# Kernel optimization log

Measured on AMD Instinct MI355X. Metric: run time of the kernel, lower is better.

Reference implementation:

```python
import jax, jax.numpy as jnp
import numpy as np

# Mamba2 dims (match init_kwargs)
DM = 1024          # d_model
EXPAND = 2
D_INNER = EXPAND * DM            # 2048 (== d_ssm)
HEADDIM = 64
NHEADS = D_INNER // HEADDIM      # 32
DSTATE = 128
NGROUPS = 1
DCONV = 4
CONV_DIM = D_INNER + 2 * NGROUPS * DSTATE        # 2304
D_IN_PROJ = 2 * D_INNER + 2 * NGROUPS * DSTATE + NHEADS  # 4384
BATCH, SEQ = 4, 1024
EPS = 1e-5


def setup_inputs() -> dict:
    key = jax.random.key(0)
    ks = jax.random.split(key, 8)
    x = jax.random.normal(ks[0], (BATCH, SEQ, DM), dtype=jnp.float32)
    in_proj_w = jax.random.normal(ks[1], (D_IN_PROJ, DM), dtype=jnp.float32) * 0.02
    conv_w = jax.random.normal(ks[2], (CONV_DIM, 1, DCONV), dtype=jnp.float32) * 0.2
    conv_b = jnp.zeros((CONV_DIM,), dtype=jnp.float32)
    # dt_bias = inv_softplus(dt) with dt ~ logU[dt_min, dt_max]
    dt = jnp.exp(jax.random.uniform(ks[3], (NHEADS,)) * (np.log(0.1) - np.log(0.001)) + np.log(0.001))
    dt_bias = dt + jnp.log(-jnp.expm1(-dt))
    # A ~ U[1, 16], A_log = log(A)
    A_log = jnp.log(jax.random.uniform(ks[4], (NHEADS,), minval=1.0, maxval=16.0))
    D = jnp.ones((NHEADS,), dtype=jnp.float32)
    norm_w = jnp.ones((D_INNER,), dtype=jnp.float32)
    out_proj_w = jax.random.normal(ks[5], (DM, D_INNER), dtype=jnp.float32) * 0.02
    return {"x": x, "in_proj_w": in_proj_w, "conv_w": conv_w, "conv_b": conv_b,
            "dt_bias": dt_bias, "A_log": A_log, "D": D, "norm_w": norm_w,
            "out_proj_w": out_proj_w}


def _mamba2_forward(x, in_proj_w, conv_w, conv_b, dt_bias, A_log, D, norm_w, out_proj_w):
    B, L, _ = x.shape
    zxbcdt = jnp.einsum('bld,ed->ble', x, in_proj_w)  # (B,L,D_IN_PROJ)
    z = zxbcdt[..., :D_INNER]
    xBC = zxbcdt[..., D_INNER:D_INNER + CONV_DIM]
    dt_raw = zxbcdt[..., D_INNER + CONV_DIM:]         # (B,L,NHEADS)

    # causal depthwise conv1d + silu
    xt = jnp.transpose(xBC, (0, 2, 1))                # (B, CONV_DIM, L)
    conv = jax.lax.conv_general_dilated(
        xt, conv_w, window_strides=(1,), padding=[(DCONV - 1, 0)],
        dimension_numbers=('NCH', 'OIH', 'NCH'), feature_group_count=CONV_DIM)
    conv = conv + conv_b[None, :, None]
    xBC = jnp.transpose(jax.nn.silu(conv), (0, 2, 1))  # (B,L,CONV_DIM)

    x_ssm = xBC[..., :D_INNER].reshape(B, L, NHEADS, HEADDIM)
    Bm = xBC[..., D_INNER:D_INNER + NGROUPS * DSTATE].reshape(B, L, NGROUPS, DSTATE)
    Cm = xBC[..., D_INNER + NGROUPS * DSTATE:].reshape(B, L, NGROUPS, DSTATE)

    dt = jax.nn.softplus(dt_raw + dt_bias)            # (B,L,H)
    A = -jnp.exp(A_log)                               # (H,)
    dA = jnp.exp(dt * A)                              # (B,L,H)
    dtx = dt[..., None] * x_ssm                       # (B,L,H,P)

    rep = NHEADS // NGROUPS
    Bh = jnp.repeat(Bm, rep, axis=2)                  # (B,L,H,N)
    Ch = jnp.repeat(Cm, rep, axis=2)

    def step(h, inp):
        dA_t, dtx_t, B_t, C_t = inp
        h = dA_t[:, :, None, None] * h + dtx_t[..., None] * B_t[:, :, None, :]
        y = jnp.einsum('bhpn,bhn->bhp', h, C_t)
        return h, y

    h0 = jnp.zeros((B, NHEADS, HEADDIM, DSTATE), dtype=x.dtype)
    xs = (jnp.transpose(dA, (1, 0, 2)),
          jnp.transpose(dtx, (1, 0, 2, 3)),
          jnp.transpose(Bh, (1, 0, 2, 3)),
          jnp.transpose(Ch, (1, 0, 2, 3)))
    _, ys = jax.lax.scan(step, h0, xs)                # (L,B,H,P)
    y = jnp.transpose(ys, (1, 0, 2, 3)) + D[None, None, :, None] * x_ssm
    y = y.reshape(B, L, D_INNER)

    # gated RMSNorm (norm_before_gate=False): normalize(y * silu(z)) * w
    yz = y * jax.nn.silu(z)
    yz = yz * jax.lax.rsqrt(jnp.mean(yz * yz, axis=-1, keepdims=True) + EPS) * norm_w

    return jnp.einsum('bld,ed->ble', yz, out_proj_w)  # (B,L,DM)


def reference(x, in_proj_w, conv_w, conv_b, dt_bias, A_log, D, norm_w, out_proj_w):
    return _mamba2_forward(x, in_proj_w, conv_w, conv_b, dt_bias, A_log, D, norm_w, out_proj_w)
```

## Files before the change

### kernel.cpp

```cpp
#include <hip/hip_runtime.h>
#include <hip/hip_bf16.h>

#define DM        1024
#define D_INNER   2048
#define NHEADS    32
#define HEADDIM   64
#define DSTATE    128
#define DCONV     4
#define CONV_DIM  (D_INNER + 2*DSTATE)
#define D_IN_PROJ (2*D_INNER + 2*DSTATE + NHEADS)
#define NPAD_IN   4480
#define BATCH     4
#define SEQ       1024
#define NROWS     (BATCH*SEQ)
#define EPSF      1e-5f
#define CHUNK     128
#define NCHUNK    (SEQ/CHUNK)
#define BH        (BATCH*NHEADS)

#define OFF_ZX   ((size_t)0)
#define OFF_XBC  ((size_t)(NROWS)*D_IN_PROJ)
#define OFF_DT   (OFF_XBC + (size_t)NROWS*CONV_DIM)
#define OFF_DA   (OFF_DT  + (size_t)NROWS*NHEADS)
#define OFF_Y    (OFF_DA  + (size_t)NROWS*NHEADS)
#define FLOAT_END (OFF_Y + (size_t)NROWS*D_INNER)
#define SOFF_XB   ((size_t)0)
#define SOFF_W1B  (SOFF_XB  + (size_t)NROWS*DM)
#define SOFF_W2B  (SOFF_W1B + (size_t)NPAD_IN*DM)
#define SOFF_YZB  (SOFF_W2B + (size_t)DM*D_INNER)
#define HD_SHORTS ((size_t)NCHUNK*BH*HEADDIM*DSTATE)

typedef float  vf4   __attribute__((ext_vector_type(4)));
typedef short  s16x8 __attribute__((ext_vector_type(8)));
typedef short  s16x4 __attribute__((ext_vector_type(4)));
typedef __bf16 bf16x8 __attribute__((ext_vector_type(8)));

__device__ __forceinline__ float sigmoidf_(float x) { return 1.f / (1.f + expf(-x)); }

__device__ __forceinline__ short f2bf(float f) {
    unsigned u = __builtin_bit_cast(unsigned, f);
    u += 0x7fffu + ((u >> 16) & 1u);
    return (short)(u >> 16);
}
__device__ __forceinline__ float bf2f(short s) {
    unsigned u = ((unsigned)(unsigned short)s) << 16;
    return __builtin_bit_cast(float, u);
}
__device__ __forceinline__ bf16x8 as_bf(s16x8 v) { return __builtin_bit_cast(bf16x8, v); }
#define MFMA(a,b,c) __builtin_amdgcn_mfma_f32_16x16x32_bf16(as_bf(a), as_bf(b), (c), 0, 0, 0)

template <typename T> __device__ __forceinline__ T cvt_out(float v);
template <> __device__ __forceinline__ float cvt_out<float>(float v) { return v; }
template <> __device__ __forceinline__ short cvt_out<short>(float v) { return f2bf(v); }

__device__ __forceinline__ void gload16(const short* g, short* l) {
    __builtin_amdgcn_global_load_lds(
        (const __attribute__((address_space(1))) unsigned int*)g,
        (__attribute__((address_space(3))) unsigned int*)l, 16, 0, 0);
}

__device__ __forceinline__ int swz_idx(int r, int kc) {
    return r * 128 + (((kc) ^ (r & 7)) << 3);
}
__device__ __forceinline__ int swz64_idx(int r, int c) {
    return r * 64 + (((c) ^ (r & 7)) << 3);
}
__device__ __forceinline__ void stage_tile(const float* __restrict__ g, int gstride,
                                           short* __restrict__ lds, int rows,
                                           int tid, int nthr) {
    for (int s = tid; s < rows * 16; s += nthr) {
        int r = s >> 4, c = s & 15;
        const float* p = g + (size_t)r * gstride + c * 8;
        float4 v0 = *(const float4*)p, v1 = *(const float4*)(p + 4);
        s16x8 o;
        o[0]=f2bf(v0.x); o[1]=f2bf(v0.y); o[2]=f2bf(v0.z); o[3]=f2bf(v0.w);
        o[4]=f2bf(v1.x); o[5]=f2bf(v1.y); o[6]=f2bf(v1.z); o[7]=f2bf(v1.w);
        *(s16x8*)&lds[swz_idx(r, c)] = o;
    }
}

__global__ __launch_bounds__(256) void cvt_bf16(const float* __restrict__ src,
                                                short* __restrict__ dst,
                                                int n_src, int n_dst) {
    int i = (blockIdx.x * 256 + threadIdx.x) * 4;
    if (i >= n_dst) return;
    s16x4 o;
    if (i + 3 < n_src) {
        float4 v = *(const float4*)(src + i);
        o[0] = f2bf(v.x); o[1] = f2bf(v.y); o[2] = f2bf(v.z); o[3] = f2bf(v.w);
    } else {
        #pragma unroll
        for (int j = 0; j < 4; ++j) o[j] = (i + j < n_src) ? f2bf(src[i + j]) : (short)0;
    }
    *(s16x4*)(dst + i) = o;
}

template <typename OutT>
__global__ __launch_bounds__(256) void gemm_mfma(const short* __restrict__ A,
                                                 const short* __restrict__ B,
                                                 OutT* __restrict__ C,
                                                 int K, int Nout, int nbx) {
    __shared__ short smem[16384];
    const int tid = threadIdx.x;
    const int cpx = gridDim.x >> 3;
    const int wgid = (blockIdx.x & 7) * cpx + (blockIdx.x >> 3);
    const int bm = (wgid / nbx) * 128, bn = (wgid % nbx) * 128;
    const int lane = tid & 63, lr = lane & 15, lg = lane >> 4;
    const int w = tid >> 6, wm = w >> 1, wn = w & 1;

    const short* ga[4]; const short* gb[4];
    short* la[4]; short* lb[4];
    #pragma unroll
    for (int t = 0; t < 4; ++t) {
        int s = t * 256 + tid;
        int r = s >> 3;
        int c = (s & 7) ^ (r & 7);
        ga[t] = A + (size_t)(bm + r) * K + c * 8;
        gb[t] = B + (size_t)(bn + r) * K + c * 8;
        la[t] = &smem[s * 8];
        lb[t] = &smem[8192 + s * 8];
    }

    vf4 acc[4][4] = {};

    for (int k0 = 0; k0 < K; k0 += 64) {
        __syncthreads();
        #pragma unroll
        for (int t = 0; t < 4; ++t) gload16(ga[t] + k0, la[t]);
        #pragma unroll
        for (int t = 0; t < 4; ++t) gload16(gb[t] + k0, lb[t]);
        __syncthreads();
        #pragma unroll
        for (int kk = 0; kk < 2; ++kk) {
            const int co = ((kk * 4 + lg) ^ (lr & 7)) * 8;
            s16x8 av[4], bv[4];
            #pragma unroll
            for (int f = 0; f < 4; ++f) {
                av[f] = *(const s16x8*)&smem[(wm * 64 + f * 16 + lr) * 64 + co];
                bv[f] = *(const s16x8*)&smem[8192 + (wn * 64 + f * 16 + lr) * 64 + co];
            }
            #pragma unroll
            for (int i = 0; i < 4; ++i)
                #pragma unroll
                for (int j = 0; j < 4; ++j)
                    acc[i][j] = MFMA(av[i], bv[j], acc[i][j]);
        }
    }

    #pragma unroll
    for (int i = 0; i < 4; ++i) {
        int row = bm + wm * 64 + i * 16 + lg * 4;
        #pragma unroll
        for (int j = 0; j < 4; ++j) {
            int col = bn + wn * 64 + j * 16 + lr;
            if (col < Nout) {
                OutT* cp = C + (size_t)row * Nout + col;
                #pragma unroll
                for (int q = 0; q < 4; ++q) cp[(size_t)q * Nout] = cvt_out<OutT>(acc[i][j][q]);
            }
        }
    }
}

__global__ __launch_bounds__(256) void conv_silu(const short* __restrict__ zx,
                                                 const float* __restrict__ cw,
                                                 const float* __restrict__ cb,
                                                 float* __restrict__ xBC) {
    int idx = blockIdx.x * 256 + threadIdx.x;
    if (idx >= NROWS * CONV_DIM) return;
    int c  = idx % CONV_DIM;
    int bl = idx / CONV_DIM;
    int b  = bl / SEQ;
    int l  = bl % SEQ;

    float w0 = cw[c*4+0], w1 = cw[c*4+1], w2 = cw[c*4+2], w3 = cw[c*4+3];
    const short* base = zx + (size_t)b * SEQ * D_IN_PROJ + D_INNER + c;

    float acc = cb[c];
    if (l >= 3) acc = fmaf(bf2f(base[(size_t)(l-3) * D_IN_PROJ]), w0, acc);
    if (l >= 2) acc = fmaf(bf2f(base[(size_t)(l-2) * D_IN_PROJ]), w1, acc);
    if (l >= 1) acc = fmaf(bf2f(base[(size_t)(l-1) * D_IN_PROJ]), w2, acc);
    acc = fmaf(bf2f(base[(size_t)l * D_IN_PROJ]), w3, acc);

    xBC[idx] = acc * sigmoidf_(acc);
}

__global__ __launch_bounds__(256) void dt_da(const short* __restrict__ zx,
                                             const float* __restrict__ dt_bias,
                                             float* __restrict__ dt) {
    int idx = blockIdx.x * 256 + threadIdx.x;
    if (idx >= NROWS * NHEADS) return;
    int h  = idx & (NHEADS - 1);
    int bl = idx >> 5;
    float u = bf2f(zx[(size_t)bl * D_IN_PROJ + D_INNER + CONV_DIM + h]) + dt_bias[h];
    float d = (u > 20.f) ? u : log1pf(expf(u));
    dt[idx] = d;
}

#define L_CT 0
#define L_XT 0
#define L_BT 16384
#define L_BW 32768
#define L_XN 49152
__global__ __launch_bounds__(1024) void ssm_mfma_a(const float* __restrict__ xBC,
                                                   const float* __restrict__ dt,
                                                   const float* __restrict__ A_log,
                                                   const float* __restrict__ Dp,
                                                   float* __restrict__ y,
                                                   short* __restrict__ hd16,
                                                   float* __restrict__ datot) {
    __shared__ short sm[57344];
    __shared__ float dtl[128], lcs[128];
    int blk = (blockIdx.x & 7) * (gridDim.x >> 3) + (blockIdx.x >> 3);
    int h = blk & 31, k = (blk >> 5) & (NCHUNK - 1), b = blk >> 8;
    int tid = threadIdx.x, w = tid >> 6, lane = tid & 63, lr = lane & 15, lg = lane >> 4;
    int bl0 = b * SEQ + k * CHUNK;
    const float* xrow = xBC + (size_t)bl0 * CONV_DIM;

    if (tid < 128) dtl[tid] = dt[(size_t)(bl0 + tid) * NHEADS + h];

    stage_tile(xrow + D_INNER + DSTATE, CONV_DIM, sm + L_CT, 128, tid, 1024);
    stage_tile(xrow + D_INNER,          CONV_DIM, sm + L_BT, 128, tid, 1024);
    {
        int r = tid >> 3, c = tid & 7;
        const float* p = xrow + (size_t)r * CONV_DIM + h * HEADDIM + c * 8;
        float4 v0 = *(const float4*)p, v1 = *(const float4*)(p + 4);
        s16x8 o;
        o[0]=f2bf(v0.x); o[1]=f2bf(v0.y); o[2]=f2bf(v0.z); o[3]=f2bf(v0.w);
        o[4]=f2bf(v1.x); o[5]=f2bf(v1.y); o[6]=f2bf(v1.z); o[7]=f2bf(v1.w);
        *(s16x8*)&sm[L_XN + swz64_idx(r, c)] = o;
    }
    __syncthreads();

    float Ah = -__expf(A_log[h]);
    if (w == 0) {
        float a = dtl[lane], bb = dtl[64 + lane];
        #pragma unroll
        for (int d = 1; d < 64; d <<= 1) { float v = __shfl_up(a, d);  if (lane >= d) a  += v; }
        #pragma unroll
        for (int d = 1; d < 64; d <<= 1) { float v = __shfl_up(bb, d); if (lane >= d) bb += v; }
        bb += __shfl(a, 63);
        lcs[lane]      = Ah * a;
        lcs[64 + lane] = Ah * bb;
        if (lane == 63) datot[k * BH + b * NHEADS + h] = __expf(Ah * bb);
    }

    vf4 g[4] = {};
    const int rb = (w & 7) * 16, cb = (w >> 3) * 64;
    #pragma unroll
    for (int ks = 0; ks < 4; ++ks) {
        int kc = ks * 4 + lg;
        s16x8 av = *(const s16x8*)&sm[L_CT + swz_idx(rb + lr, kc)];
        #pragma unroll
        for (int jf = 0; jf < 4; ++jf) {
            s16x8 bv = *(const s16x8*)&sm[L_BT + swz_idx(cb + jf * 16 + lr, kc)];
            g[jf] = MFMA(av, bv, g[jf]);
        }
    }
    __syncthreads();

    float lcLast = lcs[127];

    {
        int p = tid & 63, c2 = tid >> 6;
        s16x8 o;
        #pragma unroll
        for (int jj = 0; jj < 8; ++jj) {
            int j = c2 * 8 + jj;
            float xv = bf2f(sm[L_XN + swz64_idx(j, p >> 3) + (p & 7)]);
            o[jj] = f2bf(dtl[j] * xv);
        }
        *(s16x8*)&sm[L_XT + swz_idx(p, c2)] = o;
    }
    for (int s = tid; s < 2048; s += 1024) {
        int n = s & 127, c = s >> 7;
        s16x8 o;
        #pragma unroll
        for (int jj = 0; jj < 8; ++jj) {
            int j = c * 8 + jj;
            float bv = bf2f(sm[L_BT + swz_idx(j, n >> 3) + (n & 7)]);
            o[jj] = f2bf(bv * __expf(lcLast - lcs[j]));
        }
        *(s16x8*)&sm[L_BW + swz_idx(n, c)] = o;
    }
    __syncthreads();

    #pragma unroll
    for (int jf = 0; jf < 4; ++jf)
        #pragma unroll
        for (int q = 0; q < 4; ++q) {
            int t = rb + lg * 4 + q;
            int j = cb + jf * 16 + lr;
            float v = (j <= t) ? g[jf][q] * __expf(lcs[t] - lcs[j]) : 0.f;
            sm[L_BT + swz_idx(t, j >> 3) + (j & 7)] = f2bf(v);
        }
    __syncthreads();

    vf4 yi[2] = {};
    vf4 hdl[2] = {};
    const int rb2 = (w & 7) * 16, prb = (w >> 3) * 32;
    const int hrb = (w & 3) * 16, hcb = (w >> 2) * 32;
    #pragma unroll
    for (int ks = 0; ks < 4; ++ks) {
        int kc = ks * 4 + lg;
        s16x8 am = *(const s16x8*)&sm[L_BT + swz_idx(rb2 + lr, kc)];
        s16x8 ax = *(const s16x8*)&sm[L_XT + swz_idx(hrb + lr, kc)];
        #pragma unroll
        for (int jf = 0; jf < 2; ++jf) {
            s16x8 bx = *(const s16x8*)&sm[L_XT + swz_idx(prb + jf * 16 + lr, kc)];
            s16x8 bw = *(const s16x8*)&sm[L_BW + swz_idx(hcb + jf * 16 + lr, kc)];
            yi[jf]  = MFMA(am, bx, yi[jf]);
            hdl[jf] = MFMA(ax, bw, hdl[jf]);
        }
    }

    float Dh = Dp[h];
    #pragma unroll
    for (int jf = 0; jf < 2; ++jf)
        #pragma unroll
        for (int q = 0; q < 4; ++q) {
            int t = rb2 + lg * 4 + q;
            int p = prb + jf * 16 + lr;
            float xv = xrow[(size_t)t * CONV_DIM + h * HEADDIM + p];
            y[(size_t)(bl0 + t) * D_INNER + h * HEADDIM + p] = yi[jf][q] + Dh * xv;
        }
    size_t hb = ((size_t)k * BH + b * NHEADS + h) * (HEADDIM * DSTATE);
    #pragma unroll
    for (int jf = 0; jf < 2; ++jf)
        #pragma unroll
        for (int q = 0; q < 4; ++q) {
            int p = hrb + lg * 4 + q;
            int n = hcb + jf * 16 + lr;
            hd16[hb + p * DSTATE + n] = f2bf(hdl[jf][q]);
        }
}

__global__ __launch_bounds__(512) void ssm_state_b(short* __restrict__ hd16,
                                                   const float* __restrict__ datot) {
    int bh = blockIdx.x;
    int base = threadIdx.x * 16;
    float hs[16];
    #pragma unroll
    for (int i = 0; i < 16; ++i) hs[i] = 0.f;
    #pragma unroll
    for (int k = 0; k < NCHUNK; ++k) {
        size_t off = ((size_t)k * BH + bh) * (HEADDIM * DSTATE) + base;
        float da = datot[k * BH + bh];
        s16x8 d0 = *(const s16x8*)&hd16[off], d1 = *(const s16x8*)&hd16[off + 8];
        s16x8 o0, o1;
        #pragma unroll
        for (int i = 0; i < 8; ++i) { o0[i] = f2bf(hs[i]); o1[i] = f2bf(hs[8 + i]); }
        *(s16x8*)&hd16[off] = o0; *(s16x8*)&hd16[off + 8] = o1;
        #pragma unroll
        for (int i = 0; i < 8; ++i) {
            hs[i]     = fmaf(da, hs[i],     bf2f(d0[i]));
            hs[8 + i] = fmaf(da, hs[8 + i], bf2f(d1[i]));
        }
    }
}

__global__ __launch_bounds__(512) void ssm_mfma_c(const float* __restrict__ xBC,
                                                  const float* __restrict__ dt,
                                                  const float* __restrict__ A_log,
                                                  const short* __restrict__ hd16,
                                                  float* __restrict__ y) {
    int blk = (blockIdx.x & 7) * (gridDim.x >> 3) + (blockIdx.x >> 3);
    int h = blk & 31, k = (blk >> 5) & (NCHUNK - 1), b = blk >> 8;
    if (k == 0) return;
    __shared__ short sm[16384];
    __shared__ float dtl[128], lcs[128];
    int tid = threadIdx.x, w = tid >> 6, lane = tid & 63, lr = lane & 15, lg = lane >> 4;
    int bl0 = b * SEQ + k * CHUNK;
    const float* xrow = xBC + (size_t)bl0 * CONV_DIM;

    if (tid < 128) dtl[tid] = dt[(size_t)(bl0 + tid) * NHEADS + h];
    __syncthreads();
    stage_tile(xrow + D_INNER + DSTATE, CONV_DIM, sm, 128, tid, 512);
    float Ah = -__expf(A_log[h]);
    __syncthreads();
    if (w == 0) {
        float a = dtl[lane], bb = dtl[64 + lane];
        #pragma unroll
        for (int d = 1; d < 64; d <<= 1) { float v = __shfl_up(a, d);  if (lane >= d) a  += v; }
        #pragma unroll
        for (int d = 1; d < 64; d <<= 1) { float v = __shfl_up(bb, d); if (lane >= d) bb += v; }
        bb += __shfl(a, 63);
        lcs[lane]      = Ah * a;
        lcs[64 + lane] = Ah * bb;
    }
    __syncthreads();

    const short* hin = hd16 + ((size_t)k * BH + b * NHEADS + h) * (HEADDIM * DSTATE);
    vf4 yi[2][2] = {};
    const int rb = (w & 3) * 32, prb = (w >> 2) * 32;
    #pragma unroll
    for (int ks = 0; ks < 4; ++ks) {
        int kc = ks * 4 + lg;
        s16x8 av[2], bv[2];
        #pragma unroll
        for (int i = 0; i < 2; ++i)  { int r = rb + i * 16 + lr; av[i] = *(const s16x8*)&sm[swz_idx(r, kc)]; }
        #pragma unroll
        for (int jf = 0; jf < 2; ++jf){
            int p = prb + jf * 16 + lr;
            bv[jf] = *(const s16x8*)&hin[p * DSTATE + ks * 32 + lg * 8];
        }
        #pragma unroll
        for (int i = 0; i < 2; ++i)
            #pragma unroll
            for (int jf = 0; jf < 2; ++jf)
                yi[i][jf] = MFMA(av[i], bv[jf], yi[i][jf]);
    }
    #pragma unroll
    for (int i = 0; i < 2; ++i)
        #pragma unroll
        for (int jf = 0; jf < 2; ++jf)
            #pragma unroll
            for (int q = 0; q < 4; ++q) {
                int t = rb + i * 16 + lg * 4 + q;
                int p = prb + jf * 16 + lr;
                float* yp = y + (size_t)(bl0 + t) * D_INNER + h * HEADDIM + p;
                *yp = fmaf(__expf(lcs[t]), yi[i][jf][q], *yp);
            }
}

__global__ __launch_bounds__(256) void gate_rmsnorm(const float* __restrict__ y,
                                                    const short* __restrict__ zxs,
                                                    const float* __restrict__ nw,
                                                    short* __restrict__ yzb) {
    int bl = blockIdx.x;
    const float* yr = y + (size_t)bl * D_INNER;
    const short* zr = zxs + (size_t)bl * D_IN_PROJ;
    int e0 = threadIdx.x * 8;

    float4 y0 = *(const float4*)(yr + e0);
    float4 y1 = *(const float4*)(yr + e0 + 4);
    s16x8 zv = *(const s16x8*)(zr + e0);

    float v[8];
    float yy[8] = {y0.x, y0.y, y0.z, y0.w, y1.x, y1.y, y1.z, y1.w};
    float ss = 0.f;
    #pragma unroll
    for (int i = 0; i < 8; ++i) {
        float zz = bf2f(zv[i]);
        v[i] = yy[i] * zz * sigmoidf_(zz);
        ss = fmaf(v[i], v[i], ss);
    }
    ss += __shfl_xor(ss, 1);  ss += __shfl_xor(ss, 2);  ss += __shfl_xor(ss, 4);
    ss += __shfl_xor(ss, 8);  ss += __shfl_xor(ss, 16); ss += __shfl_xor(ss, 32);
    __shared__ float red[4];
    int wave = threadIdx.x >> 6;
    if ((threadIdx.x & 63) == 0) red[wave] = ss;
    __syncthreads();
    ss = red[0] + red[1] + red[2] + red[3];

    float scale = rsqrtf(ss * (1.f / D_INNER) + EPSF);
    s16x8 o;
    #pragma unroll
    for (int i = 0; i < 8; ++i) o[i] = f2bf(v[i] * scale * nw[e0 + i]);
    *(s16x8*)(yzb + (size_t)bl * D_INNER + e0) = o;
}

extern "C" void kernel_launch(void* const* d_in, const int* in_sizes, int n_in,
                              void* d_out, int out_size, void* d_ws, size_t ws_size,
                              hipStream_t stream) {
    const float* x        = (const float*)d_in[0];
    const float* in_w     = (const float*)d_in[1];
    const float* conv_w   = (const float*)d_in[2];
    const float* conv_b   = (const float*)d_in[3];
    const float* dt_bias  = (const float*)d_in[4];
    const float* A_log    = (const float*)d_in[5];
    const float* Dp       = (const float*)d_in[6];
    const float* norm_w   = (const float*)d_in[7];
    const float* out_w    = (const float*)d_in[8];
    float* out            = (float*)d_out;

    float* ws   = (float*)d_ws;
    short* zxs  = (short*)(ws + OFF_ZX);
    float* xBC  = ws + OFF_XBC;
    float* dt   = ws + OFF_DT;
    float* y    = ws + OFF_Y;
    short* sb   = (short*)(ws + FLOAT_END);
    short* xb   = sb + SOFF_XB;
    short* w1b  = sb + SOFF_W1B;
    short* w2b  = sb + SOFF_W2B;
    short* yzb  = sb + SOFF_YZB;
    short* hd16  = xb;
    float* datot = (float*)(hd16 + HD_SHORTS);

    {
        int n = NROWS * DM;
        cvt_bf16<<<n / 4 / 256, 256, 0, stream>>>(x, xb, n, n);
        int ns = D_IN_PROJ * DM, nd = NPAD_IN * DM;
        cvt_bf16<<<nd / 4 / 256, 256, 0, stream>>>(in_w, w1b, ns, nd);
        int n2 = DM * D_INNER;
        cvt_bf16<<<n2 / 4 / 256, 256, 0, stream>>>(out_w, w2b, n2, n2);
    }
    gemm_mfma<short><<<(NPAD_IN / 128) * (NROWS / 128), 256, 0, stream>>>(
        xb, w1b, zxs, DM, D_IN_PROJ, NPAD_IN / 128);
    {
        int total = NROWS * CONV_DIM;
        conv_silu<<<(total + 255) / 256, 256, 0, stream>>>(zxs, conv_w, conv_b, xBC);
    }
    {
        int total = NROWS * NHEADS;
        dt_da<<<(total + 255) / 256, 256, 0, stream>>>(zxs, dt_bias, dt);
    }
    ssm_mfma_a<<<BATCH * NCHUNK * NHEADS, 1024, 0, stream>>>(xBC, dt, A_log, Dp, y, hd16, datot);
    ssm_state_b<<<BH, 512, 0, stream>>>(hd16, datot);
    ssm_mfma_c<<<BATCH * NCHUNK * NHEADS, 512, 0, stream>>>(xBC, dt, A_log, hd16, y);
    gate_rmsnorm<<<NROWS, 256, 0, stream>>>(y, zxs, norm_w, yzb);
    gemm_mfma<float><<<(DM / 128) * (NROWS / 128), 256, 0, stream>>>(
        yzb, w2b, out, D_INNER, DM, DM / 128);
}
```

Measured before the change: 309.1 us.

## Store conv output as bf16, stage via direct LDS loads, split-K out_proj

The conv+SiLU output is now written as bf16 rather than fp32. The SSM kernels stage their B, C and x tiles straight into LDS with global_load_lds instead of converting fp32 to bf16 in registers, which halves that intermediate traffic. The output projection GEMM is split into two K-halves across 512 workgroups so the GPU is better filled, and a new reduce kernel sums the two partial results. This adds an extra partial buffer write/read and one more launch, and the residual x term now uses bf16-rounded values.

```diff
diff --git a/kernel.cpp b/kernel.cpp
--- a/kernel.cpp
+++ b/kernel.cpp
@@ -19,6 +19,7 @@
 #define BH        (BATCH*NHEADS)
 
 #define OFF_ZX   ((size_t)0)
+#define OFF_PART (OFF_ZX + (size_t)NROWS*D_IN_PROJ/2)
 #define OFF_XBC  ((size_t)(NROWS)*D_IN_PROJ)
 #define OFF_DT   (OFF_XBC + (size_t)NROWS*CONV_DIM)
 #define OFF_DA   (OFF_DT  + (size_t)NROWS*NHEADS)
@@ -65,19 +66,6 @@
 __device__ __forceinline__ int swz64_idx(int r, int c) {
     return r * 64 + (((c) ^ (r & 7)) << 3);
 }
-__device__ __forceinline__ void stage_tile(const float* __restrict__ g, int gstride,
-                                           short* __restrict__ lds, int rows,
-                                           int tid, int nthr) {
-    for (int s = tid; s < rows * 16; s += nthr) {
-        int r = s >> 4, c = s & 15;
-        const float* p = g + (size_t)r * gstride + c * 8;
-        float4 v0 = *(const float4*)p, v1 = *(const float4*)(p + 4);
-        s16x8 o;
-        o[0]=f2bf(v0.x); o[1]=f2bf(v0.y); o[2]=f2bf(v0.z); o[3]=f2bf(v0.w);
-        o[4]=f2bf(v1.x); o[5]=f2bf(v1.y); o[6]=f2bf(v1.z); o[7]=f2bf(v1.w);
-        *(s16x8*)&lds[swz_idx(r, c)] = o;
-    }
-}
 
 __global__ __launch_bounds__(256) void cvt_bf16(const float* __restrict__ src,
                                                 short* __restrict__ dst,
@@ -99,12 +87,15 @@
 __global__ __launch_bounds__(256) void gemm_mfma(const short* __restrict__ A,
                                                  const short* __restrict__ B,
                                                  OutT* __restrict__ C,
-                                                 int K, int Nout, int nbx) {
+                                                 int Ksplit, int Kfull, int Nout,
+                                                 int nbx, int ntiles, size_t cstride) {
     __shared__ short smem[16384];
     const int tid = threadIdx.x;
     const int cpx = gridDim.x >> 3;
     const int wgid = (blockIdx.x & 7) * cpx + (blockIdx.x >> 3);
-    const int bm = (wgid / nbx) * 128, bn = (wgid % nbx) * 128;
+    const int kz = wgid / ntiles, t2 = wgid % ntiles;
+    const int bm = (t2 / nbx) * 128, bn = (t2 % nbx) * 128;
+    const int koff = kz * Ksplit;
     const int lane = tid & 63, lr = lane & 15, lg = lane >> 4;
     const int w = tid >> 6, wm = w >> 1, wn = w & 1;
 
@@ -115,15 +106,15 @@
         int s = t * 256 + tid;
         int r = s >> 3;
         int c = (s & 7) ^ (r & 7);
-        ga[t] = A + (size_t)(bm + r) * K + c * 8;
-        gb[t] = B + (size_t)(bn + r) * K + c * 8;
+        ga[t] = A + (size_t)(bm + r) * Kfull + c * 8;
+        gb[t] = B + (size_t)(bn + r) * Kfull + c * 8;
         la[t] = &smem[s * 8];
         lb[t] = &smem[8192 + s * 8];
     }
 
     vf4 acc[4][4] = {};
 
-    for (int k0 = 0; k0 < K; k0 += 64) {
+    for (int k0 = koff; k0 < koff + Ksplit; k0 += 64) {
         __syncthreads();
         #pragma unroll
         for (int t = 0; t < 4; ++t) gload16(ga[t] + k0, la[t]);
@@ -154,7 +145,7 @@
         for (int j = 0; j < 4; ++j) {
             int col = bn + wn * 64 + j * 16 + lr;
             if (col < Nout) {
-                OutT* cp = C + (size_t)row * Nout + col;
+                OutT* cp = C + cstride * kz + (size_t)row * Nout + col;
                 #pragma unroll
                 for (int q = 0; q < 4; ++q) cp[(size_t)q * Nout] = cvt_out<OutT>(acc[i][j][q]);
             }
@@ -162,10 +153,20 @@
     }
 }
 
+__global__ __launch_bounds__(256) void reduce_add(const float* __restrict__ p,
+                                                  float* __restrict__ out, int n) {
+    int i = (blockIdx.x * 256 + threadIdx.x) * 4;
+    if (i >= n) return;
+    float4 a = *(const float4*)(p + i);
+    float4 b = *(const float4*)(p + n + i);
+    float4 o = make_float4(a.x + b.x, a.y + b.y, a.z + b.z, a.w + b.w);
+    *(float4*)(out + i) = o;
+}
+
 __global__ __launch_bounds__(256) void conv_silu(const short* __restrict__ zx,
                                                  const float* __restrict__ cw,
                                                  const float* __restrict__ cb,
-                                                 float* __restrict__ xBC) {
+                                                 short* __restrict__ xBCs) {
     int idx = blockIdx.x * 256 + threadIdx.x;
     if (idx >= NROWS * CONV_DIM) return;
     int c  = idx % CONV_DIM;
@@ -182,7 +183,7 @@
     if (l >= 1) acc = fmaf(bf2f(base[(size_t)(l-1) * D_IN_PROJ]), w2, acc);
     acc = fmaf(bf2f(base[(size_t)l * D_IN_PROJ]), w3, acc);
 
-    xBC[idx] = acc * sigmoidf_(acc);
+    xBCs[idx] = f2bf(acc * sigmoidf_(acc));
 }
 
 __global__ __launch_bounds__(256) void dt_da(const short* __restrict__ zx,
@@ -202,7 +203,7 @@
 #define L_BT 16384
 #define L_BW 32768
 #define L_XN 49152
-__global__ __launch_bounds__(1024) void ssm_mfma_a(const float* __restrict__ xBC,
+__global__ __launch_bounds__(1024) void ssm_mfma_a(const short* __restrict__ xBCs,
                                                    const float* __restrict__ dt,
                                                    const float* __restrict__ A_log,
                                                    const float* __restrict__ Dp,
@@ -215,21 +216,23 @@
     int h = blk & 31, k = (blk >> 5) & (NCHUNK - 1), b = blk >> 8;
     int tid = threadIdx.x, w = tid >> 6, lane = tid & 63, lr = lane & 15, lg = lane >> 4;
     int bl0 = b * SEQ + k * CHUNK;
-    const float* xrow = xBC + (size_t)bl0 * CONV_DIM;
-
+    const short* xrow = xBCs + (size_t)bl0 * CONV_DIM;
+
+    #pragma unroll
+    for (int t = 0; t < 2; ++t) {
+        int s = t * 1024 + tid, r = s >> 4, c = (s & 15) ^ (r & 7);
+        gload16(xrow + (size_t)r * CONV_DIM + (D_INNER + DSTATE) + c * 8, &sm[L_CT + s * 8]);
+    }
+    #pragma unroll
+    for (int t = 0; t < 2; ++t) {
+        int s = t * 1024 + tid, r = s >> 4, c = (s & 15) ^ (r & 7);
+        gload16(xrow + (size_t)r * CONV_DIM + D_INNER + c * 8, &sm[L_BT + s * 8]);
+    }
+    {
+        int r = tid >> 3, c = (tid & 7) ^ (r & 7);
+        gload16(xrow + (size_t)r * CONV_DIM + h * HEADDIM + c * 8, &sm[L_XN + tid * 8]);
+    }
     if (tid < 128) dtl[tid] = dt[(size_t)(bl0 + tid) * NHEADS + h];
-
-    stage_tile(xrow + D_INNER + DSTATE, CONV_DIM, sm + L_CT, 128, tid, 1024);
-    stage_tile(xrow + D_INNER,          CONV_DIM, sm + L_BT, 128, tid, 1024);
-    {
-        int r = tid >> 3, c = tid & 7;
-        const float* p = xrow + (size_t)r * CONV_DIM + h * HEADDIM + c * 8;
-        float4 v0 = *(const float4*)p, v1 = *(const float4*)(p + 4);
-        s16x8 o;
-        o[0]=f2bf(v0.x); o[1]=f2bf(v0.y); o[2]=f2bf(v0.z); o[3]=f2bf(v0.w);
-        o[4]=f2bf(v1.x); o[5]=f2bf(v1.y); o[6]=f2bf(v1.z); o[7]=f2bf(v1.w);
-        *(s16x8*)&sm[L_XN + swz64_idx(r, c)] = o;
-    }
     __syncthreads();
 
     float Ah = -__expf(A_log[h]);
@@ -321,7 +324,7 @@
         for (int q = 0; q < 4; ++q) {
             int t = rb2 + lg * 4 + q;
             int p = prb + jf * 16 + lr;
-            float xv = xrow[(size_t)t * CONV_DIM + h * HEADDIM + p];
+            float xv = bf2f(xrow[(size_t)t * CONV_DIM + h * HEADDIM + p]);
             y[(size_t)(bl0 + t) * D_INNER + h * HEADDIM + p] = yi[jf][q] + Dh * xv;
         }
     size_t hb = ((size_t)k * BH + b * NHEADS + h) * (HEADDIM * DSTATE);
@@ -359,7 +362,7 @@
     }
 }
 
-__global__ __launch_bounds__(512) void ssm_mfma_c(const float* __restrict__ xBC,
+__global__ __launch_bounds__(512) void ssm_mfma_c(const short* __restrict__ xBCs,
                                                   const float* __restrict__ dt,
                                                   const float* __restrict__ A_log,
                                                   const short* __restrict__ hd16,
@@ -371,11 +374,14 @@
     __shared__ float dtl[128], lcs[128];
     int tid = threadIdx.x, w = tid >> 6, lane = tid & 63, lr = lane & 15, lg = lane >> 4;
     int bl0 = b * SEQ + k * CHUNK;
-    const float* xrow = xBC + (size_t)bl0 * CONV_DIM;
-
+    const short* xrow = xBCs + (size_t)bl0 * CONV_DIM;
+
+    #pragma unroll
+    for (int t = 0; t < 4; ++t) {
+        int s = t * 512 + tid, r = s >> 4, c = (s & 15) ^ (r & 7);
+        gload16(xrow + (size_t)r * CONV_DIM + (D_INNER + DSTATE) + c * 8, &sm[s * 8]);
+    }
     if (tid < 128) dtl[tid] = dt[(size_t)(bl0 + tid) * NHEADS + h];
-    __syncthreads();
-    stage_tile(xrow + D_INNER + DSTATE, CONV_DIM, sm, 128, tid, 512);
     float Ah = -__expf(A_log[h]);
     __syncthreads();
     if (w == 0) {
@@ -476,7 +482,8 @@
 
     float* ws   = (float*)d_ws;
     short* zxs  = (short*)(ws + OFF_ZX);
-    float* xBC  = ws + OFF_XBC;
+    float* part = ws + OFF_PART;
+    short* xBCs = (short*)(ws + OFF_XBC);
     float* dt   = ws + OFF_DT;
     float* y    = ws + OFF_Y;
     short* sb   = (short*)(ws + FLOAT_END);
@@ -496,19 +503,20 @@
         cvt_bf16<<<n2 / 4 / 256, 256, 0, stream>>>(out_w, w2b, n2, n2);
     }
     gemm_mfma<short><<<(NPAD_IN / 128) * (NROWS / 128), 256, 0, stream>>>(
-        xb, w1b, zxs, DM, D_IN_PROJ, NPAD_IN / 128);
+        xb, w1b, zxs, DM, DM, D_IN_PROJ, NPAD_IN / 128, (NPAD_IN / 128) * (NROWS / 128), 0);
     {
         int total = NROWS * CONV_DIM;
-        conv_silu<<<(total + 255) / 256, 256, 0, stream>>>(zxs, conv_w, conv_b, xBC);
+        conv_silu<<<(total + 255) / 256, 256, 0, stream>>>(zxs, conv_w, conv_b, xBCs);
     }
     {
         int total = NROWS * NHEADS;
         dt_da<<<(total + 255) / 256, 256, 0, stream>>>(zxs, dt_bias, dt);
     }
-    ssm_mfma_a<<<BATCH * NCHUNK * NHEADS, 1024, 0, stream>>>(xBC, dt, A_log, Dp, y, hd16, datot);
+    ssm_mfma_a<<<BATCH * NCHUNK * NHEADS, 1024, 0, stream>>>(xBCs, dt, A_log, Dp, y, hd16, datot);
     ssm_state_b<<<BH, 512, 0, stream>>>(hd16, datot);
-    ssm_mfma_c<<<BATCH * NCHUNK * NHEADS, 512, 0, stream>>>(xBC, dt, A_log, hd16, y);
+    ssm_mfma_c<<<BATCH * NCHUNK * NHEADS, 512, 0, stream>>>(xBCs, dt, A_log, hd16, y);
     gate_rmsnorm<<<NROWS, 256, 0, stream>>>(y, zxs, norm_w, yzb);
-    gemm_mfma<float><<<(DM / 128) * (NROWS / 128), 256, 0, stream>>>(
-        yzb, w2b, out, D_INNER, DM, DM / 128);
-}
+    gemm_mfma<float><<<512, 256, 0, stream>>>(
+        yzb, w2b, part, D_INNER / 2, D_INNER, DM, DM / 128, 256, (size_t)NROWS * DM);
+    reduce_add<<<NROWS * DM / 4 / 256, 256, 0, stream>>>(part, out, NROWS * DM);
+}
```

After: 292.1 us. 1.06x faster.
